# Kernel optimization log

Measured on AMD Instinct MI355X. Metric: run time of the kernel, lower is better.

Reference implementation:

```python
import jax, jax.numpy as jnp
import numpy as np

N_NODES = 100000
N_EDGES = 6400000


def setup_inputs() -> dict:
    key = jax.random.key(0)
    k1, k2, k3, k4, k5, k6 = jax.random.split(key, 6)
    edge_predictions = jax.random.normal(k1, (N_EDGES,), dtype=jnp.float32)
    node_predictions = jax.random.normal(k2, (N_NODES,), dtype=jnp.float32)
    x = jax.random.uniform(k3, (N_NODES, 4), dtype=jnp.float32)  # col 2 = demand
    capacity = jnp.ones((1,), dtype=jnp.float32) * 50.0  # vehicle capacity
    y_edges = (jax.random.uniform(k4, (N_EDGES,)) < 0.1).astype(jnp.float32)
    y_nodes = jax.random.normal(k5, (N_NODES,), dtype=jnp.float32)
    edge_index = jax.random.randint(k6, (2, N_EDGES), 0, N_NODES, dtype=jnp.int64)
    return {
        'edge_predictions': edge_predictions,
        'node_predictions': node_predictions,
        'x': x,
        'capacity': capacity,
        'y_edges': y_edges,
        'y_nodes': y_nodes,
        'edge_index': edge_index,
        'num_nodes': N_NODES,
    }


def _bce_with_logits(logits, targets):
    # numerically stable elementwise BCE-with-logits
    return jnp.maximum(logits, 0.0) - logits * targets + jnp.log1p(jnp.exp(-jnp.abs(logits)))


def _focal_loss(logits, targets, alpha=0.25, gamma=2.0):
    bce = _bce_with_logits(logits, targets)
    probs = jax.nn.sigmoid(logits)
    p_t = probs * targets + (1.0 - probs) * (1.0 - targets)
    alpha_t = alpha * targets + (1.0 - alpha) * (1.0 - targets)
    return jnp.mean(alpha_t * (1.0 - p_t) ** gamma * bce)


def reference(edge_predictions, node_predictions, x, capacity, y_edges, y_nodes,
              edge_index, num_nodes):
    edge_probs = jax.nn.sigmoid(edge_predictions)
    src, dst = edge_index[0], edge_index[1]

    # single segment-sum pass over edges replaces the O(num_nodes * num_edges) loops
    in_sums = jax.ops.segment_sum(edge_probs, dst, num_segments=num_nodes)   # [N]
    out_sums = jax.ops.segment_sum(edge_probs, src, num_segments=num_nodes)  # [N]

    # coverage loss: customer nodes (1..N-1) should have in/out degree-prob == 1
    coverage = (jnp.sum((in_sums[1:] - 1.0) ** 2) + jnp.sum((out_sums[1:] - 1.0) ** 2)) \
               / (2.0 * max(num_nodes - 1, 1))

    # tour formation: flow conservation over ALL nodes
    tour_formation = jnp.sum((in_sums - out_sums) ** 2) / num_nodes

    # depot balance
    depot_balance = (in_sums[0] - out_sums[0]) ** 2

    # capacity tours: depot out-degree ~ ceil(total_demand / capacity)
    demands = x[:, 2]
    total_demand = jnp.sum(demands[1:])
    cap_value = jax.lax.stop_gradient(jnp.mean(capacity))  # torch uses .item()
    expected_tours = jnp.ceil(total_demand / cap_value)
    capacity_tours = (out_sums[0] - expected_tours) ** 2

    # similarity (focal) loss on raw logits
    similarity = _focal_loss(edge_predictions, y_edges, alpha=0.25, gamma=2.0)

    # masked node MSE (mask is data-dependent -> where-based mean)
    mask = (y_nodes >= 0.0).astype(node_predictions.dtype)
    cnt = jnp.maximum(jnp.sum(mask), 1.0)
    node_loss = jnp.sum(mask * (node_predictions - y_nodes) ** 2) / cnt

    total = (coverage * 5.0 + tour_formation * 3.0 + depot_balance * 2.0 +
             capacity_tours * 1.5 + similarity * 0.3 + node_loss * 0.1)
    return total
```

## Files before the change

kernel.cpp:

```cpp
#include <hip/hip_runtime.h>
#include <math.h>

#define RANGE_LOG 8
#define RANGE 256
#define NB_META 512
#define CAP 34400u
#define EDGES_PER_CHUNK 4096
#define SCAT_THREADS 512
#define EPT 8
#define PARTS 4



__device__ __forceinline__ float wave_reduce_sum(float v) {
    #pragma unroll
    for (int o = 32; o > 0; o >>= 1) v += __shfl_down(v, o, 64);
    return v;
}

template <int NW>
__device__ float block_reduce_sum(float v) {
    __shared__ float s[NW];
    __syncthreads();
    const int lane = threadIdx.x & 63;
    const int wid  = threadIdx.x >> 6;
    v = wave_reduce_sum(v);
    if (lane == 0) s[wid] = v;
    __syncthreads();
    float r = 0.f;
    if (wid == 0) {
        float x = (lane < NW) ? s[lane] : 0.f;
        r = wave_reduce_sum(x);
    }
    return r;
}

#define LOG2E 1.44269504f
#define LN2   0.69314718f

__device__ __forceinline__ float fast_focal(float x, float t, float& p) {
    const float ax = fabsf(x);
    const float e  = __builtin_amdgcn_exp2f(-ax * LOG2E);
    const float r  = __builtin_amdgcn_rcpf(1.f + e);
    p = (x >= 0.f) ? r : 1.f - r;
    const float sp  = __builtin_amdgcn_logf(1.f + e) * LN2;
    const float bce = fmaxf(x, 0.f) - x * t + sp;
    const float p_t = p * t + (1.f - p) * (1.f - t);
    const float a_t = 0.25f * t + 0.75f * (1.f - t);
    const float om  = 1.f - p_t;
    return a_t * om * om * bce;
}


__global__ __launch_bounds__(SCAT_THREADS, 8)
void scatter_kernel(const float* __restrict__ ep,
                    const float* __restrict__ ye,
                    const int*   __restrict__ ei,
                    unsigned* __restrict__ cursor,
                    unsigned short* __restrict__ pairs,
                    float* __restrict__ acc,
                    int E) {
    __shared__ unsigned s_hist[NB_META];
    __shared__ unsigned s_off[NB_META];
    __shared__ unsigned s_gbase[NB_META];
    __shared__ unsigned s_pack[2 * EDGES_PER_CHUNK];

    const int tid   = threadIdx.x;
    const int lane  = tid & 63;
    const int wid   = tid >> 6;
    const int ebase = blockIdx.x * EDGES_PER_CHUNK;
    const int ec    = min(EDGES_PER_CHUNK, E - ebase);
    const int cnt   = 2 * ec;

    s_hist[tid] = 0u;
    __syncthreads();

    unsigned pk[2 * EPT];
    unsigned rkp[EPT];
    float local = 0.f;
    const int  le0  = tid * EPT;
    const bool full = (le0 + EPT) <= ec;

    if (full) {
        const int e0 = ebase + le0;
        #pragma unroll
        for (int h = 0; h < 2; ++h) {
            const float4 xv = *(const float4*)(ep + e0 + 4 * h);
            const float4 tv = *(const float4*)(ye + e0 + 4 * h);
            const int4   sv = *(const int4*)(ei + e0 + 4 * h);
            const int4   dv = *(const int4*)(ei + E + e0 + 4 * h);
            const float xx[4] = {xv.x, xv.y, xv.z, xv.w};
            const float tt[4] = {tv.x, tv.y, tv.z, tv.w};
            const unsigned ss[4] = {(unsigned)sv.x, (unsigned)sv.y, (unsigned)sv.z, (unsigned)sv.w};
            const unsigned dd[4] = {(unsigned)dv.x, (unsigned)dv.y, (unsigned)dv.z, (unsigned)dv.w};
            #pragma unroll
            for (int j = 0; j < 4; ++j) {
                float p;
                local += fast_focal(xx[j], tt[j], p);
                const unsigned pq = min((unsigned)(p * 128.f + 0.5f), 127u);
                const int k = 4 * h + j;
                const unsigned sb = ss[j] >> RANGE_LOG, db = dd[j] >> RANGE_LOG;
                pk[2 * k]     = (sb << 16) | ((ss[j] & (RANGE - 1)) << 8) | pq;
                pk[2 * k + 1] = (db << 16) | ((dd[j] & (RANGE - 1)) << 8) | 128u | pq;
                const unsigned r0 = atomicAdd(&s_hist[sb], 1u);
                const unsigned r1 = atomicAdd(&s_hist[db], 1u);
                rkp[k] = r0 | (r1 << 16);
            }
        }
    } else {
        #pragma unroll
        for (int k = 0; k < EPT; ++k) {
            pk[2 * k] = 0xFFFFFFFFu;
            pk[2 * k + 1] = 0xFFFFFFFFu;
            rkp[k] = 0u;
            const int el = le0 + k;
            if (el < ec) {
                const int e = ebase + el;
                float p;
                local += fast_focal(ep[e], ye[e], p);
                const unsigned pq = min((unsigned)(p * 128.f + 0.5f), 127u);
                const unsigned s = (unsigned)ei[e];
                const unsigned d = (unsigned)ei[E + e];
                const unsigned sb = s >> RANGE_LOG, db = d >> RANGE_LOG;
                pk[2 * k]     = (sb << 16) | ((s & (RANGE - 1)) << 8) | pq;
                pk[2 * k + 1] = (db << 16) | ((d & (RANGE - 1)) << 8) | 128u | pq;
                const unsigned r0 = atomicAdd(&s_hist[sb], 1u);
                const unsigned r1 = atomicAdd(&s_hist[db], 1u);
                rkp[k] = r0 | (r1 << 16);
            }
        }
    }
    __syncthreads();

    const unsigned h = s_hist[tid];
    unsigned v = h;
    #pragma unroll
    for (int o = 1; o < 64; o <<= 1) {
        const unsigned t = (unsigned)__shfl_up((int)v, o, 64);
        if (lane >= o) v += t;
    }
    if (lane == 63) s_gbase[wid] = v;
    __syncthreads();
    if (wid == 0 && lane < 8) {
        unsigned x = s_gbase[lane];
        #pragma unroll
        for (int o = 1; o < 8; o <<= 1) {
            const unsigned t = (unsigned)__shfl_up((int)x, o, 8);
            if (lane >= o) x += t;
        }
        s_gbase[lane] = x;
    }
    __syncthreads();
    const unsigned wbase = (wid > 0) ? s_gbase[wid - 1] : 0u;
    __syncthreads();
    const unsigned excl = wbase + v - h;
    s_off[tid]   = excl;
    s_gbase[tid] = h ? (atomicAdd(&cursor[tid], h) - excl) : 0u;
    __syncthreads();

    if (full) {
        #pragma unroll
        for (int k = 0; k < 2 * EPT; ++k) {
            const unsigned pv = pk[k];
            const unsigned r  = (rkp[k >> 1] >> ((k & 1) * 16)) & 0xFFFFu;
            s_pack[s_off[pv >> 16] + r] = pv;
        }
    } else {
        #pragma unroll
        for (int k = 0; k < 2 * EPT; ++k) {
            const unsigned pv = pk[k];
            if (pv != 0xFFFFFFFFu) {
                const unsigned r = (rkp[k >> 1] >> ((k & 1) * 16)) & 0xFFFFu;
                s_pack[s_off[pv >> 16] + r] = pv;
            }
        }
    }
    __syncthreads();

    for (int idx = tid; idx < cnt; idx += SCAT_THREADS) {
        const unsigned pv = s_pack[idx];
        const unsigned b  = pv >> 16;
        pairs[(size_t)b * CAP + (unsigned)(s_gbase[b] + (unsigned)idx)] =
            (unsigned short)pv;
    }

    const float bs = block_reduce_sum<SCAT_THREADS / 64>(local);
    if (tid == 0) atomicAdd(&acc[0], bs);
}

__global__ __launch_bounds__(256, 8)
void accum_kernel(const unsigned* __restrict__ cursor,
                  const unsigned short* __restrict__ pairs,
                  unsigned* __restrict__ partials,
                  int N, int nbuck) {
    __shared__ unsigned sAcc[4 * RANGE];
    const int tid  = threadIdx.x;
    const int par  = tid & 1;
    const int b    = blockIdx.x % nbuck;
    const int part = blockIdx.x / nbuck;
    #pragma unroll
    for (int i = 0; i < 4; ++i) sAcc[tid + 256 * i] = 0u;
    __syncthreads();

    unsigned fill = cursor[b];
    if (fill > CAP) fill = CAP;
    const unsigned lo = ((unsigned)(((unsigned long long)fill * part) / PARTS)) & ~7u;
    const unsigned hi = (part == PARTS - 1)
        ? fill
        : (((unsigned)(((unsigned long long)fill * (part + 1)) / PARTS)) & ~7u);
    const size_t gb = (size_t)b * CAP;
    const unsigned hiv = lo + ((hi - lo) & ~7u);

    for (unsigned i = lo + 8 * tid; i < hiv; i += 8 * 256) {
        const uint4 v = *(const uint4*)(pairs + gb + i);
        const unsigned d0 = v.x, d1 = v.y, d2 = v.z, d3 = v.w;
        atomicAdd(&sAcc[((((d0 & 0xFFFFu) >> 7) << 1) | par)], d0 & 127u);
        atomicAdd(&sAcc[(((d0 >> 23) << 1) | par)], (d0 >> 16) & 127u);
        atomicAdd(&sAcc[((((d1 & 0xFFFFu) >> 7) << 1) | par)], d1 & 127u);
        atomicAdd(&sAcc[(((d1 >> 23) << 1) | par)], (d1 >> 16) & 127u);
        atomicAdd(&sAcc[((((d2 & 0xFFFFu) >> 7) << 1) | par)], d2 & 127u);
        atomicAdd(&sAcc[(((d2 >> 23) << 1) | par)], (d2 >> 16) & 127u);
        atomicAdd(&sAcc[((((d3 & 0xFFFFu) >> 7) << 1) | par)], d3 & 127u);
        atomicAdd(&sAcc[(((d3 >> 23) << 1) | par)], (d3 >> 16) & 127u);
    }
    for (unsigned i = hiv + tid; i < hi; i += 256) {
        const unsigned u = pairs[gb + i];
        atomicAdd(&sAcc[(((u >> 7) << 1) | par)], u & 127u);
    }
    __syncthreads();

    const int nodes = min(RANGE, N - b * RANGE);
    unsigned* dstp = partials + (size_t)part * 2 * N + 2 * (size_t)(b * RANGE);
    for (int i = tid; i < nodes; i += 256) {
        const unsigned outv = sAcc[(i << 2)] + sAcc[(i << 2) | 1];
        const unsigned inv  = sAcc[(i << 2) | 2] + sAcc[(i << 2) | 3];
        uint2 w; w.x = outv; w.y = inv;
        *(uint2*)(dstp + 2 * i) = w;
    }
}

__global__ void node_cov3_kernel(const float* __restrict__ npred,
                                 const float* __restrict__ yn,
                                 const float* __restrict__ x,
                                 const unsigned* __restrict__ partials,
                                 float* __restrict__ acc,
                                 const float* __restrict__ capacity,
                                 float* __restrict__ out,
                                 unsigned* __restrict__ done,
                                 int N, int E) {
    __shared__ bool is_last;
    const int i = blockIdx.x * blockDim.x + threadIdx.x;
    float dem = 0.f, cntm = 0.f, sq = 0.f, cov = 0.f, tour = 0.f;
    if (i < N) {
        unsigned ou = 0u, iu = 0u;
        #pragma unroll
        for (int p = 0; p < PARTS; ++p) {
            const uint2 v = *(const uint2*)(partials + (size_t)p * 2 * N + 2 * (size_t)i);
            ou += v.x;
            iu += v.y;
        }
        const float outv = (float)ou * (1.f / 128.f);
        const float inv  = (float)iu * (1.f / 128.f);
        if (i >= 1) dem = x[i * 4 + 2];
        const float y = yn[i];
        if (y >= 0.f) {
            cntm = 1.f;
            const float d = npred[i] - y;
            sq = d * d;
        }
        const float dd = inv - outv;
        tour = dd * dd;
        if (i >= 1) cov = (inv - 1.f) * (inv - 1.f) + (outv - 1.f) * (outv - 1.f);
        if (i == 0) { atomicAdd(&acc[6], inv); atomicAdd(&acc[7], outv); }
    }
    float r;
    r = block_reduce_sum<4>(dem);  if (threadIdx.x == 0) atomicAdd(&acc[1], r);
    r = block_reduce_sum<4>(cntm); if (threadIdx.x == 0) atomicAdd(&acc[2], r);
    r = block_reduce_sum<4>(sq);   if (threadIdx.x == 0) atomicAdd(&acc[3], r);
    r = block_reduce_sum<4>(cov);  if (threadIdx.x == 0) atomicAdd(&acc[4], r);
    r = block_reduce_sum<4>(tour); if (threadIdx.x == 0) atomicAdd(&acc[5], r);

    if (threadIdx.x == 0) {
        __threadfence();
        const unsigned t = atomicAdd(done, 1u);
        is_last = (t == (unsigned)(gridDim.x - 1));
    }
    __syncthreads();
    if (is_last && threadIdx.x == 0) {
        __threadfence();
        const float coverage = acc[4] / (2.0f * (float)(N - 1));
        const float tourv    = acc[5] / (float)N;
        const float in0  = acc[6];
        const float out0 = acc[7];
        const float depot = (in0 - out0) * (in0 - out0);
        const float cap = capacity[0];
        const float expected = ceilf(acc[1] / cap);
        const float cap_t = (out0 - expected) * (out0 - expected);
        const float sim = acc[0] / (float)E;
        const float node_loss = acc[3] / fmaxf(acc[2], 1.f);
        out[0] = coverage * 5.f + tourv * 3.f + depot * 2.f + cap_t * 1.5f +
                 sim * 0.3f + node_loss * 0.1f;
    }
}


__global__ void edge_kernel(const float* __restrict__ ep,
                            const float* __restrict__ ye,
                            const int*   __restrict__ src,
                            const int*   __restrict__ dst,
                            float* __restrict__ in_sums,
                            float* __restrict__ out_sums,
                            float* __restrict__ acc,
                            int E) {
    float local = 0.f;
    for (int i = blockIdx.x * blockDim.x + threadIdx.x; i < E;
         i += gridDim.x * blockDim.x) {
        const float x = ep[i];
        float p;
        local += fast_focal(x, ye[i], p);
        unsafeAtomicAdd(&out_sums[src[i]], p);
        unsafeAtomicAdd(&in_sums[dst[i]], p);
    }
    const float bs = block_reduce_sum<4>(local);
    if (threadIdx.x == 0) atomicAdd(&acc[0], bs);
}

__global__ void node_cov_kernel(const float* __restrict__ npred,
                                const float* __restrict__ yn,
                                const float* __restrict__ x,
                                const float* __restrict__ in_sums,
                                const float* __restrict__ out_sums,
                                float* __restrict__ acc,
                                const float* __restrict__ capacity,
                                float* __restrict__ out,
                                unsigned* __restrict__ done,
                                int N, int E) {
    __shared__ bool is_last;
    const int i = blockIdx.x * blockDim.x + threadIdx.x;
    float dem = 0.f, cntm = 0.f, sq = 0.f, cov = 0.f, tour = 0.f;
    if (i < N) {
        if (i >= 1) dem = x[i * 4 + 2];
        const float y = yn[i];
        if (y >= 0.f) {
            cntm = 1.f;
            const float d = npred[i] - y;
            sq = d * d;
        }
        const float a = in_sums[i];
        const float b = out_sums[i];
        const float dd = a - b;
        tour = dd * dd;
        if (i >= 1) cov = (a - 1.f) * (a - 1.f) + (b - 1.f) * (b - 1.f);
        if (i == 0) { atomicAdd(&acc[6], a); atomicAdd(&acc[7], b); }
    }
    float r;
    r = block_reduce_sum<4>(dem);  if (threadIdx.x == 0) atomicAdd(&acc[1], r);
    r = block_reduce_sum<4>(cntm); if (threadIdx.x == 0) atomicAdd(&acc[2], r);
    r = block_reduce_sum<4>(sq);   if (threadIdx.x == 0) atomicAdd(&acc[3], r);
    r = block_reduce_sum<4>(cov);  if (threadIdx.x == 0) atomicAdd(&acc[4], r);
    r = block_reduce_sum<4>(tour); if (threadIdx.x == 0) atomicAdd(&acc[5], r);

    if (threadIdx.x == 0) {
        __threadfence();
        const unsigned t = atomicAdd(done, 1u);
        is_last = (t == (unsigned)(gridDim.x - 1));
    }
    __syncthreads();
    if (is_last && threadIdx.x == 0) {
        __threadfence();
        const float coverage = acc[4] / (2.0f * (float)(N - 1));
        const float tourv    = acc[5] / (float)N;
        const float depot = (acc[6] - acc[7]) * (acc[6] - acc[7]);
        const float expected = ceilf(acc[1] / capacity[0]);
        const float cap_t = (acc[7] - expected) * (acc[7] - expected);
        const float sim = acc[0] / (float)E;
        const float node_loss = acc[3] / fmaxf(acc[2], 1.f);
        out[0] = coverage * 5.f + tourv * 3.f + depot * 2.f + cap_t * 1.5f +
                 sim * 0.3f + node_loss * 0.1f;
    }
}


extern "C" void kernel_launch(void* const* d_in, const int* in_sizes, int n_in,
                              void* d_out, int out_size, void* d_ws, size_t ws_size,
                              hipStream_t stream) {
    const float* ep       = (const float*)d_in[0];
    const float* npred    = (const float*)d_in[1];
    const float* x        = (const float*)d_in[2];
    const float* capacity = (const float*)d_in[3];
    const float* ye       = (const float*)d_in[4];
    const float* yn       = (const float*)d_in[5];
    const int*   ei       = (const int*)d_in[6];

    const int E = in_sizes[0];
    const int N = in_sizes[1];
    const int nbuck = (N + RANGE - 1) / RANGE;

    char* w = (char*)d_ws;
    float*    acc    = (float*)w;
    unsigned* cursor = (unsigned*)(w + 256);
    unsigned* done   = (unsigned*)(w + 3840);
    unsigned* partials = (unsigned*)(w + 4096);
    size_t off_pairs = 4096 + (size_t)PARTS * 2 * N * sizeof(unsigned);
    off_pairs = (off_pairs + 255) & ~(size_t)255;
    unsigned short* pairs = (unsigned short*)(w + off_pairs);
    const size_t need = off_pairs + (size_t)nbuck * CAP * sizeof(unsigned short) + 65536;

    if (nbuck <= NB_META && ws_size >= need && (E % 4) == 0 && N < (1 << 17)) {
        hipMemsetAsync(d_ws, 0, 4096, stream);
        const int nchunks = (E + EDGES_PER_CHUNK - 1) / EDGES_PER_CHUNK;
        scatter_kernel<<<nchunks, SCAT_THREADS, 0, stream>>>(
            ep, ye, ei, cursor, pairs, acc, E);
        accum_kernel<<<nbuck * PARTS, 256, 0, stream>>>(
            cursor, pairs, partials, N, nbuck);
        node_cov3_kernel<<<(N + 255) / 256, 256, 0, stream>>>(
            npred, yn, x, partials, acc, capacity, (float*)d_out, done, N, E);
    } else {
        float* in_sums  = (float*)(w + 4096);
        float* out_sums = in_sums + N;
        hipMemsetAsync(d_ws, 0, 4096 + (size_t)2 * N * sizeof(float), stream);
        edge_kernel<<<4096, 256, 0, stream>>>(ep, ye, ei, ei + E, in_sums,
                                              out_sums, acc, E);
        node_cov_kernel<<<(N + 255) / 256, 256, 0, stream>>>(
            npred, yn, x, in_sums, out_sums, acc, capacity, (float*)d_out,
            done, N, E);
    }
}
```

Measured before the change: 194.3 us.

## Fuse node coverage pass into accumulate kernel and derive scatter slots via LDS cursors

Removes the separate node_cov3 kernel launch. Each bucket's last-finishing part block, detected through a per-bucket atomic counter, now reduces the partials and computes the node losses, and a global counter picks the block that writes the final result. The scatter kernel no longer keeps per-edge rank registers from the histogram atomics. Instead it claims slots with a second round of LDS atomicAdds on per-bucket cursors, trading register pressure for extra shared-memory atomics. The workspace layout grows to hold the per-bucket done counters.

```diff
diff --git a/kernel.cpp b/kernel.cpp
--- a/kernel.cpp
+++ b/kernel.cpp
@@ -61,7 +61,7 @@
                     float* __restrict__ acc,
                     int E) {
     __shared__ unsigned s_hist[NB_META];
-    __shared__ unsigned s_off[NB_META];
+    __shared__ unsigned s_cur[NB_META];
     __shared__ unsigned s_gbase[NB_META];
     __shared__ unsigned s_pack[2 * EDGES_PER_CHUNK];
 
@@ -76,7 +76,6 @@
     __syncthreads();
 
     unsigned pk[2 * EPT];
-    unsigned rkp[EPT];
     float local = 0.f;
     const int  le0  = tid * EPT;
     const bool full = (le0 + EPT) <= ec;
@@ -102,9 +101,8 @@
                 const unsigned sb = ss[j] >> RANGE_LOG, db = dd[j] >> RANGE_LOG;
                 pk[2 * k]     = (sb << 16) | ((ss[j] & (RANGE - 1)) << 8) | pq;
                 pk[2 * k + 1] = (db << 16) | ((dd[j] & (RANGE - 1)) << 8) | 128u | pq;
-                const unsigned r0 = atomicAdd(&s_hist[sb], 1u);
-                const unsigned r1 = atomicAdd(&s_hist[db], 1u);
-                rkp[k] = r0 | (r1 << 16);
+                atomicAdd(&s_hist[sb], 1u);
+                atomicAdd(&s_hist[db], 1u);
             }
         }
     } else {
@@ -112,7 +110,6 @@
         for (int k = 0; k < EPT; ++k) {
             pk[2 * k] = 0xFFFFFFFFu;
             pk[2 * k + 1] = 0xFFFFFFFFu;
-            rkp[k] = 0u;
             const int el = le0 + k;
             if (el < ec) {
                 const int e = ebase + el;
@@ -124,9 +121,8 @@
                 const unsigned sb = s >> RANGE_LOG, db = d >> RANGE_LOG;
                 pk[2 * k]     = (sb << 16) | ((s & (RANGE - 1)) << 8) | pq;
                 pk[2 * k + 1] = (db << 16) | ((d & (RANGE - 1)) << 8) | 128u | pq;
-                const unsigned r0 = atomicAdd(&s_hist[sb], 1u);
-                const unsigned r1 = atomicAdd(&s_hist[db], 1u);
-                rkp[k] = r0 | (r1 << 16);
+                atomicAdd(&s_hist[sb], 1u);
+                atomicAdd(&s_hist[db], 1u);
             }
         }
     }
@@ -154,7 +150,7 @@
     const unsigned wbase = (wid > 0) ? s_gbase[wid - 1] : 0u;
     __syncthreads();
     const unsigned excl = wbase + v - h;
-    s_off[tid]   = excl;
+    s_cur[tid]   = excl;
     s_gbase[tid] = h ? (atomicAdd(&cursor[tid], h) - excl) : 0u;
     __syncthreads();
 
@@ -162,16 +158,16 @@
         #pragma unroll
         for (int k = 0; k < 2 * EPT; ++k) {
             const unsigned pv = pk[k];
-            const unsigned r  = (rkp[k >> 1] >> ((k & 1) * 16)) & 0xFFFFu;
-            s_pack[s_off[pv >> 16] + r] = pv;
+            const unsigned r = atomicAdd(&s_cur[pv >> 16], 1u);
+            s_pack[r] = pv;
         }
     } else {
         #pragma unroll
         for (int k = 0; k < 2 * EPT; ++k) {
             const unsigned pv = pk[k];
             if (pv != 0xFFFFFFFFu) {
-                const unsigned r = (rkp[k >> 1] >> ((k & 1) * 16)) & 0xFFFFu;
-                s_pack[s_off[pv >> 16] + r] = pv;
+                const unsigned r = atomicAdd(&s_cur[pv >> 16], 1u);
+                s_pack[r] = pv;
             }
         }
     }
@@ -189,11 +185,20 @@
 }
 
 __global__ __launch_bounds__(256, 8)
-void accum_kernel(const unsigned* __restrict__ cursor,
-                  const unsigned short* __restrict__ pairs,
-                  unsigned* __restrict__ partials,
-                  int N, int nbuck) {
+void accum_cov_kernel(const unsigned* __restrict__ cursor,
+                      const unsigned short* __restrict__ pairs,
+                      unsigned* __restrict__ partials,
+                      unsigned* __restrict__ bdone,
+                      unsigned* __restrict__ done,
+                      const float* __restrict__ npred,
+                      const float* __restrict__ yn,
+                      const float* __restrict__ x,
+                      const float* __restrict__ capacity,
+                      float* __restrict__ acc,
+                      float* __restrict__ out,
+                      int N, int nbuck, int E) {
     __shared__ unsigned sAcc[4 * RANGE];
+    __shared__ bool s_lastpart, s_lastall;
     const int tid  = threadIdx.x;
     const int par  = tid & 1;
     const int b    = blockIdx.x % nbuck;
@@ -234,59 +239,57 @@
     for (int i = tid; i < nodes; i += 256) {
         const unsigned outv = sAcc[(i << 2)] + sAcc[(i << 2) | 1];
         const unsigned inv  = sAcc[(i << 2) | 2] + sAcc[(i << 2) | 3];
-        uint2 w; w.x = outv; w.y = inv;
-        *(uint2*)(dstp + 2 * i) = w;
-    }
-}
-
-__global__ void node_cov3_kernel(const float* __restrict__ npred,
-                                 const float* __restrict__ yn,
-                                 const float* __restrict__ x,
-                                 const unsigned* __restrict__ partials,
-                                 float* __restrict__ acc,
-                                 const float* __restrict__ capacity,
-                                 float* __restrict__ out,
-                                 unsigned* __restrict__ done,
-                                 int N, int E) {
-    __shared__ bool is_last;
-    const int i = blockIdx.x * blockDim.x + threadIdx.x;
+        uint2 w2; w2.x = outv; w2.y = inv;
+        *(uint2*)(dstp + 2 * i) = w2;
+    }
+    __threadfence();
+    __syncthreads();
+    if (tid == 0) {
+        const unsigned t = atomicAdd(&bdone[b], 1u);
+        s_lastpart = (t == (unsigned)(PARTS - 1));
+    }
+    __syncthreads();
+    if (!s_lastpart) return;
+    __threadfence();
+
     float dem = 0.f, cntm = 0.f, sq = 0.f, cov = 0.f, tour = 0.f;
-    if (i < N) {
+    if (tid < nodes) {
+        const int g = b * RANGE + tid;
         unsigned ou = 0u, iu = 0u;
         #pragma unroll
         for (int p = 0; p < PARTS; ++p) {
-            const uint2 v = *(const uint2*)(partials + (size_t)p * 2 * N + 2 * (size_t)i);
+            const uint2 v = *(const uint2*)(partials + (size_t)p * 2 * N + 2 * (size_t)g);
             ou += v.x;
             iu += v.y;
         }
         const float outv = (float)ou * (1.f / 128.f);
         const float inv  = (float)iu * (1.f / 128.f);
-        if (i >= 1) dem = x[i * 4 + 2];
-        const float y = yn[i];
+        if (g >= 1) dem = x[g * 4 + 2];
+        const float y = yn[g];
         if (y >= 0.f) {
             cntm = 1.f;
-            const float d = npred[i] - y;
+            const float d = npred[g] - y;
             sq = d * d;
         }
         const float dd = inv - outv;
         tour = dd * dd;
-        if (i >= 1) cov = (inv - 1.f) * (inv - 1.f) + (outv - 1.f) * (outv - 1.f);
-        if (i == 0) { atomicAdd(&acc[6], inv); atomicAdd(&acc[7], outv); }
+        if (g >= 1) cov = (inv - 1.f) * (inv - 1.f) + (outv - 1.f) * (outv - 1.f);
+        if (g == 0) { atomicAdd(&acc[6], inv); atomicAdd(&acc[7], outv); }
     }
     float r;
-    r = block_reduce_sum<4>(dem);  if (threadIdx.x == 0) atomicAdd(&acc[1], r);
-    r = block_reduce_sum<4>(cntm); if (threadIdx.x == 0) atomicAdd(&acc[2], r);
-    r = block_reduce_sum<4>(sq);   if (threadIdx.x == 0) atomicAdd(&acc[3], r);
-    r = block_reduce_sum<4>(cov);  if (threadIdx.x == 0) atomicAdd(&acc[4], r);
-    r = block_reduce_sum<4>(tour); if (threadIdx.x == 0) atomicAdd(&acc[5], r);
-
-    if (threadIdx.x == 0) {
+    r = block_reduce_sum<4>(dem);  if (tid == 0) atomicAdd(&acc[1], r);
+    r = block_reduce_sum<4>(cntm); if (tid == 0) atomicAdd(&acc[2], r);
+    r = block_reduce_sum<4>(sq);   if (tid == 0) atomicAdd(&acc[3], r);
+    r = block_reduce_sum<4>(cov);  if (tid == 0) atomicAdd(&acc[4], r);
+    r = block_reduce_sum<4>(tour); if (tid == 0) atomicAdd(&acc[5], r);
+
+    if (tid == 0) {
         __threadfence();
         const unsigned t = atomicAdd(done, 1u);
-        is_last = (t == (unsigned)(gridDim.x - 1));
-    }
-    __syncthreads();
-    if (is_last && threadIdx.x == 0) {
+        s_lastall = (t == (unsigned)(nbuck - 1));
+    }
+    __syncthreads();
+    if (s_lastall && tid == 0) {
         __threadfence();
         const float coverage = acc[4] / (2.0f * (float)(N - 1));
         const float tourv    = acc[5] / (float)N;
@@ -399,26 +402,26 @@
     char* w = (char*)d_ws;
     float*    acc    = (float*)w;
     unsigned* cursor = (unsigned*)(w + 256);
-    unsigned* done   = (unsigned*)(w + 3840);
-    unsigned* partials = (unsigned*)(w + 4096);
-    size_t off_pairs = 4096 + (size_t)PARTS * 2 * N * sizeof(unsigned);
+    unsigned* bdone  = (unsigned*)(w + 2560);
+    unsigned* done   = (unsigned*)(w + 4608);
+    unsigned* partials = (unsigned*)(w + 8192);
+    size_t off_pairs = 8192 + (size_t)PARTS * 2 * N * sizeof(unsigned);
     off_pairs = (off_pairs + 255) & ~(size_t)255;
     unsigned short* pairs = (unsigned short*)(w + off_pairs);
     const size_t need = off_pairs + (size_t)nbuck * CAP * sizeof(unsigned short) + 65536;
 
     if (nbuck <= NB_META && ws_size >= need && (E % 4) == 0 && N < (1 << 17)) {
-        hipMemsetAsync(d_ws, 0, 4096, stream);
+        hipMemsetAsync(d_ws, 0, 8192, stream);
         const int nchunks = (E + EDGES_PER_CHUNK - 1) / EDGES_PER_CHUNK;
         scatter_kernel<<<nchunks, SCAT_THREADS, 0, stream>>>(
             ep, ye, ei, cursor, pairs, acc, E);
-        accum_kernel<<<nbuck * PARTS, 256, 0, stream>>>(
-            cursor, pairs, partials, N, nbuck);
-        node_cov3_kernel<<<(N + 255) / 256, 256, 0, stream>>>(
-            npred, yn, x, partials, acc, capacity, (float*)d_out, done, N, E);
+        accum_cov_kernel<<<nbuck * PARTS, 256, 0, stream>>>(
+            cursor, pairs, partials, bdone, done, npred, yn, x, capacity,
+            acc, (float*)d_out, N, nbuck, E);
     } else {
-        float* in_sums  = (float*)(w + 4096);
+        float* in_sums  = (float*)(w + 8192);
         float* out_sums = in_sums + N;
-        hipMemsetAsync(d_ws, 0, 4096 + (size_t)2 * N * sizeof(float), stream);
+        hipMemsetAsync(d_ws, 0, 8192 + (size_t)2 * N * sizeof(float), stream);
         edge_kernel<<<4096, 256, 0, stream>>>(ep, ye, ei, ei + E, in_sums,
                                               out_sums, acc, E);
         node_cov_kernel<<<(N + 255) / 256, 256, 0, stream>>>(
```

New measurement: 325.0 us. +67.2%, slower.
